# Performance work log

Measured on AMD Instinct MI355X. Metric: run time of the kernel, lower is better.

## Reference

```python
import jax, jax.numpy as jnp
import numpy as np

B, DIM, N_TREES, DEPTH, UNITS = 512, 256, 512, 6, 3
N_LEAVES = 2 ** DEPTH


def binary_lookup_table(depth):
    # (depth, 2**depth, 2) float table of leaf bit codes, as in get_binary_lookup_table
    idx = np.arange(2 ** depth)
    off = 2 ** np.arange(depth)
    bits = (idx[None, :] // off[:, None]) % 2  # (depth, 2**depth)
    lut = np.stack([bits, 1 - bits], axis=-1).astype(np.float32)
    return jnp.asarray(lut)


def sparsemax(z, axis):
    # sparsemax along `axis` (Martins & Astudillo 2016)
    z = jnp.moveaxis(z, axis, -1)
    K = z.shape[-1]
    zs = jnp.flip(jnp.sort(z, axis=-1), axis=-1)
    k = jnp.arange(1, K + 1, dtype=z.dtype)
    cum = jnp.cumsum(zs, axis=-1)
    support = (1.0 + k * zs) > cum
    k_z = jnp.sum(support, axis=-1, keepdims=True)  # int
    tau_num = jnp.take_along_axis(cum, k_z - 1, axis=-1) - 1.0
    tau = tau_num / k_z.astype(z.dtype)
    out = jnp.maximum(z - tau, 0.0)
    return jnp.moveaxis(out, -1, axis)


def sparsemoid(t):
    return jnp.clip(0.5 * t + 0.5, 0.0, 1.0)


def setup_inputs() -> dict:
    key = jax.random.key(0)
    k1, k2, k3, k4 = jax.random.split(key, 4)
    return {
        "x": jax.random.normal(k1, (B, DIM), dtype=jnp.float32),
        "feature_selection_logits": jax.random.normal(k2, (DIM, N_TREES, DEPTH), dtype=jnp.float32),
        "feature_thresholds": jax.random.normal(k3, (N_TREES, DEPTH), dtype=jnp.float32) * 0.5,
        "log_temperatures": jnp.zeros((N_TREES, DEPTH), dtype=jnp.float32),
        "response": jax.random.normal(k4, (N_TREES, UNITS, N_LEAVES), dtype=jnp.float32),
    }


def reference(x, feature_selection_logits, feature_thresholds, log_temperatures, response):
    depth = feature_thresholds.shape[-1]
    lut = binary_lookup_table(depth)  # (d, 2**d, 2) constant
    # soft feature selection: sparsemax over the feature dimension i
    selectors = sparsemax(feature_selection_logits, axis=0)  # (i, n, d)
    fv = jnp.einsum('bi,ind->bnd', x, selectors)  # (b, n, d)
    # binary gates
    tl = (fv - feature_thresholds) * jnp.exp(-log_temperatures)  # (b, n, d)
    gates = sparsemoid(jnp.stack([-tl, tl], axis=-1))  # (b, n, d, 2)
    # leaf aggregation: product over depth of per-level gate selected by the leaf bit code
    agg = jnp.einsum('bnds,dcs->bndc', gates, lut)  # (b, n, d, 2**d)
    leaf_probs = jnp.prod(agg, axis=-2)  # (b, n, 2**d)
    out = jnp.einsum('bnc,nuc->bnu', leaf_probs, response)  # (b, n, units)
    return out
```

## Files before the change

### kernel.cpp

```cpp
#include <hip/hip_runtime.h>
#include <hip/hip_bf16.h>

#define BATCH 512
#define DIM 256
#define NT 512
#define DEPTH 6
#define UNITS 3
#define NL 64
#define COLS (NT * DEPTH)
#define KMAX 32


__global__ __launch_bounds__(256) void k_pack(
    const float* __restrict__ logits, const float* __restrict__ resp,
    const float* __restrict__ thr, const float* __restrict__ ltemp,
    float* __restrict__ logitsT, float4* __restrict__ resp4,
    float* __restrict__ pth, float* __restrict__ pet) {
  const int bid = blockIdx.x, tid = threadIdx.x;
  if (bid < 192) {
    const int c0 = (bid % 48) * 64, r0 = (bid / 48) * 64;
    __shared__ float tile[64][65];
#pragma unroll
    for (int e = tid; e < 4096; e += 256) {
      int r = e >> 6, c = e & 63;
      tile[r][c] = logits[(r0 + r) * COLS + c0 + c];
    }
    __syncthreads();
#pragma unroll
    for (int e = tid; e < 4096; e += 256) {
      int c = e >> 6, r = e & 63;
      logitsT[(c0 + c) * DIM + r0 + r] = tile[r][c];
    }
  } else if (bid < 576) {
    int idx = (bid - 192) * 256 + tid;
    int n = idx / (UNITS * NL);
    int r = idx % (UNITS * NL);
    int u = r / NL, c = r % NL;
    ((float*)&resp4[c * NT + n])[u] = resp[idx];
  } else {
    int idx = (bid - 576) * 256 + tid;
    int n = idx / DEPTH, d = idx % DEPTH;
    pth[d * NT + n] = thr[idx];
    pet[d * NT + n] = expf(-ltemp[idx]);
  }
}

__global__ __launch_bounds__(256) void k_sel(
    const float* __restrict__ logitsT, float4* __restrict__ val4,
    unsigned int* __restrict__ idx4, int* __restrict__ cnt) {
  const int wv = threadIdx.x >> 6, lane = threadIdx.x & 63;
  const int col = blockIdx.x * 4 + wv;
  const int n = col / DEPTH, d = col % DEPTH;

  float z[4];
#pragma unroll
  for (int j = 0; j < 4; ++j) z[j] = logitsT[col * DIM + j * 64 + lane];

  float m = fmaxf(fmaxf(z[0], z[1]), fmaxf(z[2], z[3]));
#pragma unroll
  for (int o = 32; o > 0; o >>= 1) m = fmaxf(m, __shfl_xor(m, o, 64));

  float tau = m - 1.0f;
  for (int it = 0; it < 16; ++it) {
    float s = 0.0f, k = 0.0f;
#pragma unroll
    for (int j = 0; j < 4; ++j) {
      float dd = z[j] - tau;
      if (dd > 0.0f) { s += dd; k += 1.0f; }
    }
#pragma unroll
    for (int o = 32; o > 0; o >>= 1) {
      s += __shfl_xor(s, o, 64);
      k += __shfl_xor(k, o, 64);
    }
    float delta = (s - 1.0f) / k;
    tau += delta;
    if (fabsf(delta) < 1e-7f) break;
  }

  float* vbase = (float*)val4;
  unsigned char* ibase = (unsigned char*)idx4;
  int base = 0;
#pragma unroll
  for (int j = 0; j < 4; ++j) {
    bool nz = z[j] > tau;
    unsigned long long mk = __ballot(nz);
    int pos = base + __popcll(mk & ((1ull << lane) - 1ull));
    if (nz && pos < KMAX) {
      int slot = ((d * 8 + (pos >> 2)) * NT + n) * 4 + (pos & 3);
      vbase[slot] = z[j] - tau;
      ibase[slot] = (unsigned char)(j * 64 + lane);
    }
    base += __popcll(mk);
  }
  const int cc = min(base, KMAX);
  if (lane >= cc && lane < KMAX) {
    int slot = ((d * 8 + (lane >> 2)) * NT + n) * 4 + (lane & 3);
    vbase[slot] = 0.0f;
    ibase[slot] = 0;
  }
  if (lane == 0) cnt[d * NT + n] = cc;
}

__global__ __launch_bounds__(256) void k_forest4(
    const float* __restrict__ x, const float4* __restrict__ val4,
    const unsigned int* __restrict__ idx4, const int* __restrict__ cnt,
    const float* __restrict__ pth, const float* __restrict__ pet,
    const float4* __restrict__ resp4, float* __restrict__ out) {
  const int tid = threadIdx.x;
  const int nloc = tid & 63, bg = tid >> 6;
  const int tt = blockIdx.x & 7, bt = blockIdx.x >> 3;
  const int n = tt * 64 + nloc;
  const int b0 = bt * 8;

  __shared__ float xl[8 * DIM];
#pragma unroll
  for (int k = 0; k < 8; ++k) xl[k * 256 + tid] = x[b0 * DIM + k * 256 + tid];
  __syncthreads();

  const float* xr0 = &xl[(bg * 2 + 0) * DIM];
  const float* xr1 = &xl[(bg * 2 + 1) * DIM];

  float fv0[DEPTH], fv1[DEPTH];
#pragma unroll
  for (int d = 0; d < DEPTH; ++d) { fv0[d] = 0.0f; fv1[d] = 0.0f; }

#pragma unroll
  for (int d = 0; d < DEPTH; ++d) {
    int mc = cnt[d * NT + n];
#pragma unroll
    for (int o = 32; o > 0; o >>= 1) mc = max(mc, __shfl_xor(mc, o, 64));
    const int nq = (mc + 3) >> 2;
#pragma unroll
    for (int jq = 0; jq < 8; ++jq) {
      if (jq < nq) {
        float4 v = val4[(d * 8 + jq) * NT + n];
        unsigned int ip = idx4[(d * 8 + jq) * NT + n];
        int i0 = ip & 255, i1 = (ip >> 8) & 255;
        int i2 = (ip >> 16) & 255, i3 = ip >> 24;
        fv0[d] = fmaf(v.x, xr0[i0], fv0[d]); fv1[d] = fmaf(v.x, xr1[i0], fv1[d]);
        fv0[d] = fmaf(v.y, xr0[i1], fv0[d]); fv1[d] = fmaf(v.y, xr1[i1], fv1[d]);
        fv0[d] = fmaf(v.z, xr0[i2], fv0[d]); fv1[d] = fmaf(v.z, xr1[i2], fv1[d]);
        fv0[d] = fmaf(v.w, xr0[i3], fv0[d]); fv1[d] = fmaf(v.w, xr1[i3], fv1[d]);
      }
    }
  }

  float th[DEPTH], et[DEPTH];
#pragma unroll
  for (int d = 0; d < DEPTH; ++d) {
    th[d] = pth[d * NT + n];
    et[d] = pet[d * NT + n];
  }

  float t012[2][8], t345[2][8];
#pragma unroll
  for (int r = 0; r < 2; ++r) {
    float g0[DEPTH], g1[DEPTH];
#pragma unroll
    for (int d = 0; d < DEPTH; ++d) {
      float av = r ? fv1[d] : fv0[d];
      float tl = (av - th[d]) * et[d];
      float gg = fminf(fmaxf(0.5f * tl + 0.5f, 0.0f), 1.0f);
      g0[d] = gg;
      g1[d] = 1.0f - gg;
    }
#pragma unroll
    for (int c = 0; c < 8; ++c) {
      t012[r][c] = ((c & 1) ? g1[0] : g0[0]) * ((c & 2) ? g1[1] : g0[1]) *
                   ((c & 4) ? g1[2] : g0[2]);
      t345[r][c] = ((c & 1) ? g1[3] : g0[3]) * ((c & 2) ? g1[4] : g0[4]) *
                   ((c & 4) ? g1[5] : g0[5]);
    }
  }

  float o00 = 0, o01 = 0, o02 = 0, o10 = 0, o11 = 0, o12 = 0;
#pragma unroll
  for (int c = 0; c < NL; ++c) {
    float4 rr = resp4[c * NT + n];
    float p0 = t012[0][c & 7] * t345[0][c >> 3];
    float p1 = t012[1][c & 7] * t345[1][c >> 3];
    o00 = fmaf(p0, rr.x, o00); o01 = fmaf(p0, rr.y, o01); o02 = fmaf(p0, rr.z, o02);
    o10 = fmaf(p1, rr.x, o10); o11 = fmaf(p1, rr.y, o11); o12 = fmaf(p1, rr.z, o12);
  }

  const int ba = b0 + bg * 2, bb = ba + 1;
  float* oa = out + ((size_t)ba * NT + n) * UNITS;
  float* ob = out + ((size_t)bb * NT + n) * UNITS;
  oa[0] = o00; oa[1] = o01; oa[2] = o02;
  ob[0] = o10; ob[1] = o11; ob[2] = o12;
}

extern "C" void kernel_launch(void* const* d_in, const int* in_sizes, int n_in,
                              void* d_out, int out_size, void* d_ws, size_t ws_size,
                              hipStream_t stream) {
  const float* x    = (const float*)d_in[0];
  const float* fsl  = (const float*)d_in[1];
  const float* thr  = (const float*)d_in[2];
  const float* lt   = (const float*)d_in[3];
  const float* resp = (const float*)d_in[4];
  float* out = (float*)d_out;

  float* ws = (float*)d_ws;
  float*        logitsT = ws;
  float4*       resp4   = (float4*)(ws + 786432);
  float4*       val4    = (float4*)(ws + 917504);
  unsigned int* idx4    = (unsigned int*)(ws + 1015808);
  int*          cnt     = (int*)(ws + 1040384);
  float*        pth     = ws + 1043456;
  float*        pet     = ws + 1046528;

  k_pack<<<588, 256, 0, stream>>>(fsl, resp, thr, lt, logitsT, resp4, pth, pet);
  k_sel<<<COLS / 4, 256, 0, stream>>>(logitsT, val4, idx4, cnt);
  k_forest4<<<512, 256, 0, stream>>>(x, val4, idx4, cnt, pth, pet, resp4, out);
}
```

Measured before the change: 94.23 us.

## Fuse pack into sparsemax and forest kernels, staging response in shared memory

Removes the separate pack kernel. The sparsemax kernel now transposes the logits through a shared-memory tile itself, and the forest kernel reads thresholds, temperatures and the response table directly, staging the response transposed in LDS. The forest kernel also drops from two batch rows per thread to one and launches twice as many blocks. This cuts one launch and the global round-trips for logitsT and resp4, at the cost of each forest block reloading 48KB of response and recomputing expf per thread.

```diff
diff --git a/kernel.cpp b/kernel.cpp
--- a/kernel.cpp
+++ b/kernel.cpp
@@ -11,119 +11,106 @@
 #define KMAX 32
 
 
-__global__ __launch_bounds__(256) void k_pack(
-    const float* __restrict__ logits, const float* __restrict__ resp,
-    const float* __restrict__ thr, const float* __restrict__ ltemp,
-    float* __restrict__ logitsT, float4* __restrict__ resp4,
-    float* __restrict__ pth, float* __restrict__ pet) {
-  const int bid = blockIdx.x, tid = threadIdx.x;
-  if (bid < 192) {
-    const int c0 = (bid % 48) * 64, r0 = (bid / 48) * 64;
-    __shared__ float tile[64][65];
+__global__ __launch_bounds__(512) void k_sparse(
+    const float* __restrict__ logits, float4* __restrict__ val4,
+    unsigned int* __restrict__ idx4, int* __restrict__ cnt) {
+  const int tid = threadIdx.x;
+  const int c0 = blockIdx.x * 16;
+  __shared__ float tile[16][260];
 #pragma unroll
-    for (int e = tid; e < 4096; e += 256) {
-      int r = e >> 6, c = e & 63;
-      tile[r][c] = logits[(r0 + r) * COLS + c0 + c];
+  for (int it = 0; it < 8; ++it) {
+    int e = it * 512 + tid;
+    int r = e >> 4, c = e & 15;
+    tile[c][r] = logits[r * COLS + c0 + c];
+  }
+  __syncthreads();
+
+  const int wv = tid >> 6, lane = tid & 63;
+  float* vbase = (float*)val4;
+  unsigned char* ibase = (unsigned char*)idx4;
+
+#pragma unroll
+  for (int q = 0; q < 2; ++q) {
+    const int cl = wv * 2 + q;
+    const int col = c0 + cl;
+    const int n = col / DEPTH, d = col % DEPTH;
+
+    float z[4];
+#pragma unroll
+    for (int j = 0; j < 4; ++j) z[j] = tile[cl][j * 64 + lane];
+
+    float m = fmaxf(fmaxf(z[0], z[1]), fmaxf(z[2], z[3]));
+#pragma unroll
+    for (int o = 32; o > 0; o >>= 1) m = fmaxf(m, __shfl_xor(m, o, 64));
+
+    float tau = m - 1.0f;
+    for (int itn = 0; itn < 16; ++itn) {
+      float s = 0.0f, k = 0.0f;
+#pragma unroll
+      for (int j = 0; j < 4; ++j) {
+        float dd = z[j] - tau;
+        if (dd > 0.0f) { s += dd; k += 1.0f; }
+      }
+#pragma unroll
+      for (int o = 32; o > 0; o >>= 1) {
+        s += __shfl_xor(s, o, 64);
+        k += __shfl_xor(k, o, 64);
+      }
+      float delta = (s - 1.0f) / k;
+      tau += delta;
+      if (fabsf(delta) < 1e-7f) break;
     }
-    __syncthreads();
+
+    int base = 0;
 #pragma unroll
-    for (int e = tid; e < 4096; e += 256) {
-      int c = e >> 6, r = e & 63;
-      logitsT[(c0 + c) * DIM + r0 + r] = tile[r][c];
+    for (int j = 0; j < 4; ++j) {
+      bool nz = z[j] > tau;
+      unsigned long long mk = __ballot(nz);
+      int pos = base + __popcll(mk & ((1ull << lane) - 1ull));
+      if (nz && pos < KMAX) {
+        int slot = ((d * 8 + (pos >> 2)) * NT + n) * 4 + (pos & 3);
+        vbase[slot] = z[j] - tau;
+        ibase[slot] = (unsigned char)(j * 64 + lane);
+      }
+      base += __popcll(mk);
     }
-  } else if (bid < 576) {
-    int idx = (bid - 192) * 256 + tid;
-    int n = idx / (UNITS * NL);
-    int r = idx % (UNITS * NL);
-    int u = r / NL, c = r % NL;
-    ((float*)&resp4[c * NT + n])[u] = resp[idx];
-  } else {
-    int idx = (bid - 576) * 256 + tid;
-    int n = idx / DEPTH, d = idx % DEPTH;
-    pth[d * NT + n] = thr[idx];
-    pet[d * NT + n] = expf(-ltemp[idx]);
+    const int cc = min(base, KMAX);
+    if (lane >= cc && lane < KMAX) {
+      int slot = ((d * 8 + (lane >> 2)) * NT + n) * 4 + (lane & 3);
+      vbase[slot] = 0.0f;
+      ibase[slot] = 0;
+    }
+    if (lane == 0) cnt[d * NT + n] = cc;
   }
 }
 
-__global__ __launch_bounds__(256) void k_sel(
-    const float* __restrict__ logitsT, float4* __restrict__ val4,
-    unsigned int* __restrict__ idx4, int* __restrict__ cnt) {
-  const int wv = threadIdx.x >> 6, lane = threadIdx.x & 63;
-  const int col = blockIdx.x * 4 + wv;
-  const int n = col / DEPTH, d = col % DEPTH;
-
-  float z[4];
-#pragma unroll
-  for (int j = 0; j < 4; ++j) z[j] = logitsT[col * DIM + j * 64 + lane];
-
-  float m = fmaxf(fmaxf(z[0], z[1]), fmaxf(z[2], z[3]));
-#pragma unroll
-  for (int o = 32; o > 0; o >>= 1) m = fmaxf(m, __shfl_xor(m, o, 64));
-
-  float tau = m - 1.0f;
-  for (int it = 0; it < 16; ++it) {
-    float s = 0.0f, k = 0.0f;
-#pragma unroll
-    for (int j = 0; j < 4; ++j) {
-      float dd = z[j] - tau;
-      if (dd > 0.0f) { s += dd; k += 1.0f; }
-    }
-#pragma unroll
-    for (int o = 32; o > 0; o >>= 1) {
-      s += __shfl_xor(s, o, 64);
-      k += __shfl_xor(k, o, 64);
-    }
-    float delta = (s - 1.0f) / k;
-    tau += delta;
-    if (fabsf(delta) < 1e-7f) break;
-  }
-
-  float* vbase = (float*)val4;
-  unsigned char* ibase = (unsigned char*)idx4;
-  int base = 0;
-#pragma unroll
-  for (int j = 0; j < 4; ++j) {
-    bool nz = z[j] > tau;
-    unsigned long long mk = __ballot(nz);
-    int pos = base + __popcll(mk & ((1ull << lane) - 1ull));
-    if (nz && pos < KMAX) {
-      int slot = ((d * 8 + (pos >> 2)) * NT + n) * 4 + (pos & 3);
-      vbase[slot] = z[j] - tau;
-      ibase[slot] = (unsigned char)(j * 64 + lane);
-    }
-    base += __popcll(mk);
-  }
-  const int cc = min(base, KMAX);
-  if (lane >= cc && lane < KMAX) {
-    int slot = ((d * 8 + (lane >> 2)) * NT + n) * 4 + (lane & 3);
-    vbase[slot] = 0.0f;
-    ibase[slot] = 0;
-  }
-  if (lane == 0) cnt[d * NT + n] = cc;
-}
-
-__global__ __launch_bounds__(256) void k_forest4(
+__global__ __launch_bounds__(256) void k_forest5(
     const float* __restrict__ x, const float4* __restrict__ val4,
     const unsigned int* __restrict__ idx4, const int* __restrict__ cnt,
-    const float* __restrict__ pth, const float* __restrict__ pet,
-    const float4* __restrict__ resp4, float* __restrict__ out) {
+    const float* __restrict__ thr, const float* __restrict__ ltemp,
+    const float* __restrict__ resp, float* __restrict__ out) {
   const int tid = threadIdx.x;
   const int nloc = tid & 63, bg = tid >> 6;
   const int tt = blockIdx.x & 7, bt = blockIdx.x >> 3;
-  const int n = tt * 64 + nloc;
-  const int b0 = bt * 8;
+  const int n = tt * 64 + nloc, n0 = tt * 64;
+  const int b = bt * 4 + bg;
 
-  __shared__ float xl[8 * DIM];
+  __shared__ float xl[4 * DIM];
+  __shared__ float rsp[UNITS][NL][65];
 #pragma unroll
-  for (int k = 0; k < 8; ++k) xl[k * 256 + tid] = x[b0 * DIM + k * 256 + tid];
+  for (int k2 = 0; k2 < 4; ++k2)
+    xl[k2 * 256 + tid] = x[(bt * 4 + k2) * DIM + tid];
+  for (int k2 = 0; k2 < 48; ++k2) {
+    int e = k2 * 256 + tid;
+    int nl = e / 192, rem = e - nl * 192;
+    rsp[rem >> 6][rem & 63][nl] = resp[n0 * 192 + e];
+  }
   __syncthreads();
 
-  const float* xr0 = &xl[(bg * 2 + 0) * DIM];
-  const float* xr1 = &xl[(bg * 2 + 1) * DIM];
-
-  float fv0[DEPTH], fv1[DEPTH];
+  const float* xr = &xl[bg * DIM];
+  float fv[DEPTH];
 #pragma unroll
-  for (int d = 0; d < DEPTH; ++d) { fv0[d] = 0.0f; fv1[d] = 0.0f; }
+  for (int d = 0; d < DEPTH; ++d) fv[d] = 0.0f;
 
 #pragma unroll
   for (int d = 0; d < DEPTH; ++d) {
@@ -136,59 +123,44 @@
       if (jq < nq) {
         float4 v = val4[(d * 8 + jq) * NT + n];
         unsigned int ip = idx4[(d * 8 + jq) * NT + n];
-        int i0 = ip & 255, i1 = (ip >> 8) & 255;
-        int i2 = (ip >> 16) & 255, i3 = ip >> 24;
-        fv0[d] = fmaf(v.x, xr0[i0], fv0[d]); fv1[d] = fmaf(v.x, xr1[i0], fv1[d]);
-        fv0[d] = fmaf(v.y, xr0[i1], fv0[d]); fv1[d] = fmaf(v.y, xr1[i1], fv1[d]);
-        fv0[d] = fmaf(v.z, xr0[i2], fv0[d]); fv1[d] = fmaf(v.z, xr1[i2], fv1[d]);
-        fv0[d] = fmaf(v.w, xr0[i3], fv0[d]); fv1[d] = fmaf(v.w, xr1[i3], fv1[d]);
+        fv[d] = fmaf(v.x, xr[ip & 255], fv[d]);
+        fv[d] = fmaf(v.y, xr[(ip >> 8) & 255], fv[d]);
+        fv[d] = fmaf(v.z, xr[(ip >> 16) & 255], fv[d]);
+        fv[d] = fmaf(v.w, xr[ip >> 24], fv[d]);
       }
     }
   }
 
-  float th[DEPTH], et[DEPTH];
-#pragma unroll
-  for (int d = 0; d < DEPTH; ++d) {
-    th[d] = pth[d * NT + n];
-    et[d] = pet[d * NT + n];
-  }
-
-  float t012[2][8], t345[2][8];
-#pragma unroll
-  for (int r = 0; r < 2; ++r) {
+  float t012[8], t345[8];
+  {
     float g0[DEPTH], g1[DEPTH];
 #pragma unroll
     for (int d = 0; d < DEPTH; ++d) {
-      float av = r ? fv1[d] : fv0[d];
-      float tl = (av - th[d]) * et[d];
+      float tl = (fv[d] - thr[n * DEPTH + d]) * expf(-ltemp[n * DEPTH + d]);
       float gg = fminf(fmaxf(0.5f * tl + 0.5f, 0.0f), 1.0f);
       g0[d] = gg;
       g1[d] = 1.0f - gg;
     }
 #pragma unroll
     for (int c = 0; c < 8; ++c) {
-      t012[r][c] = ((c & 1) ? g1[0] : g0[0]) * ((c & 2) ? g1[1] : g0[1]) *
-                   ((c & 4) ? g1[2] : g0[2]);
-      t345[r][c] = ((c & 1) ? g1[3] : g0[3]) * ((c & 2) ? g1[4] : g0[4]) *
-                   ((c & 4) ? g1[5] : g0[5]);
+      t012[c] = ((c & 1) ? g1[0] : g0[0]) * ((c & 2) ? g1[1] : g0[1]) *
+                ((c & 4) ? g1[2] : g0[2]);
+      t345[c] = ((c & 1) ? g1[3] : g0[3]) * ((c & 2) ? g1[4] : g0[4]) *
+                ((c & 4) ? g1[5] : g0[5]);
     }
   }
 
-  float o00 = 0, o01 = 0, o02 = 0, o10 = 0, o11 = 0, o12 = 0;
+  float o0 = 0.0f, o1 = 0.0f, o2 = 0.0f;
 #pragma unroll
   for (int c = 0; c < NL; ++c) {
-    float4 rr = resp4[c * NT + n];
-    float p0 = t012[0][c & 7] * t345[0][c >> 3];
-    float p1 = t012[1][c & 7] * t345[1][c >> 3];
-    o00 = fmaf(p0, rr.x, o00); o01 = fmaf(p0, rr.y, o01); o02 = fmaf(p0, rr.z, o02);
-    o10 = fmaf(p1, rr.x, o10); o11 = fmaf(p1, rr.y, o11); o12 = fmaf(p1, rr.z, o12);
+    float p = t012[c & 7] * t345[c >> 3];
+    o0 = fmaf(p, rsp[0][c][nloc], o0);
+    o1 = fmaf(p, rsp[1][c][nloc], o1);
+    o2 = fmaf(p, rsp[2][c][nloc], o2);
   }
 
-  const int ba = b0 + bg * 2, bb = ba + 1;
-  float* oa = out + ((size_t)ba * NT + n) * UNITS;
-  float* ob = out + ((size_t)bb * NT + n) * UNITS;
-  oa[0] = o00; oa[1] = o01; oa[2] = o02;
-  ob[0] = o10; ob[1] = o11; ob[2] = o12;
+  float* op = out + ((size_t)b * NT + n) * UNITS;
+  op[0] = o0; op[1] = o1; op[2] = o2;
 }
 
 extern "C" void kernel_launch(void* const* d_in, const int* in_sizes, int n_in,
@@ -202,15 +174,10 @@
   float* out = (float*)d_out;
 
   float* ws = (float*)d_ws;
-  float*        logitsT = ws;
-  float4*       resp4   = (float4*)(ws + 786432);
-  float4*       val4    = (float4*)(ws + 917504);
-  unsigned int* idx4    = (unsigned int*)(ws + 1015808);
-  int*          cnt     = (int*)(ws + 1040384);
-  float*        pth     = ws + 1043456;
-  float*        pet     = ws + 1046528;
+  float4*       val4 = (float4*)ws;
+  unsigned int* idx4 = (unsigned int*)(ws + 98304);
+  int*          cnt  = (int*)(ws + 122880);
 
-  k_pack<<<588, 256, 0, stream>>>(fsl, resp, thr, lt, logitsT, resp4, pth, pet);
-  k_sel<<<COLS / 4, 256, 0, stream>>>(logitsT, val4, idx4, cnt);
-  k_forest4<<<512, 256, 0, stream>>>(x, val4, idx4, cnt, pth, pet, resp4, out);
+  k_sparse<<<COLS / 16, 512, 0, stream>>>(fsl, val4, idx4, cnt);
+  k_forest5<<<1024, 256, 0, stream>>>(x, val4, idx4, cnt, thr, lt, resp, out);
 }
```

New measurement: 98.94 us. 1.05x slower.

## Fuse transpose with sparsemax selection and store responses as bf16

Applied to the files above, without the earlier changes.

Merges the logits transpose and the sparsemax selection into a single prep kernel. Each block now loads its 8 columns through shared memory, so the logitsT round-trip through global memory and one kernel launch go away. Response weights are stored as packed bf16 (uint2 instead of float4), which halves that read in the forest kernel. The count-driven early exit is removed so all 8 quads are always processed, which adds some work on zero-padded entries. The bf16 responses reduce precision of the final output.

```diff
diff --git a/kernel.cpp b/kernel.cpp
--- a/kernel.cpp
+++ b/kernel.cpp
@@ -11,102 +11,120 @@
 #define KMAX 32
 
 
-__global__ __launch_bounds__(256) void k_pack(
+__device__ __forceinline__ unsigned short f2bf(float f) {
+  unsigned int u = __float_as_uint(f);
+  return (unsigned short)((u + 0x7fffu + ((u >> 16) & 1u)) >> 16);
+}
+
+__global__ __launch_bounds__(512) void k_prep6(
     const float* __restrict__ logits, const float* __restrict__ resp,
     const float* __restrict__ thr, const float* __restrict__ ltemp,
-    float* __restrict__ logitsT, float4* __restrict__ resp4,
-    float* __restrict__ pth, float* __restrict__ pet) {
+    float4* __restrict__ val4, unsigned int* __restrict__ idx4,
+    uint2* __restrict__ respB, float* __restrict__ pth,
+    float* __restrict__ pet) {
   const int bid = blockIdx.x, tid = threadIdx.x;
-  if (bid < 192) {
-    const int c0 = (bid % 48) * 64, r0 = (bid / 48) * 64;
-    __shared__ float tile[64][65];
-#pragma unroll
-    for (int e = tid; e < 4096; e += 256) {
-      int r = e >> 6, c = e & 63;
-      tile[r][c] = logits[(r0 + r) * COLS + c0 + c];
+  __shared__ float tile[8][260];
+  __shared__ float lds[64 * 196];
+
+  if (bid < 384) {
+    const int c0 = bid * 8;
+#pragma unroll
+    for (int it = 0; it < 4; ++it) {
+      int e = it * 512 + tid;
+      int r = e >> 3, c = e & 7;
+      tile[c][r] = logits[r * COLS + c0 + c];
     }
     __syncthreads();
-#pragma unroll
-    for (int e = tid; e < 4096; e += 256) {
-      int c = e >> 6, r = e & 63;
-      logitsT[(c0 + c) * DIM + r0 + r] = tile[r][c];
-    }
-  } else if (bid < 576) {
-    int idx = (bid - 192) * 256 + tid;
-    int n = idx / (UNITS * NL);
-    int r = idx % (UNITS * NL);
-    int u = r / NL, c = r % NL;
-    ((float*)&resp4[c * NT + n])[u] = resp[idx];
+
+    const int wv = tid >> 6, lane = tid & 63;
+    const int col = c0 + wv;
+    const int n = col / DEPTH, d = col % DEPTH;
+
+    float z[4];
+#pragma unroll
+    for (int j = 0; j < 4; ++j) z[j] = tile[wv][j * 64 + lane];
+
+    float m = fmaxf(fmaxf(z[0], z[1]), fmaxf(z[2], z[3]));
+#pragma unroll
+    for (int o = 32; o > 0; o >>= 1) m = fmaxf(m, __shfl_xor(m, o, 64));
+
+    float tau = m - 1.0f;
+    for (int itn = 0; itn < 16; ++itn) {
+      float s = 0.0f, k = 0.0f;
+#pragma unroll
+      for (int j = 0; j < 4; ++j) {
+        float dd = z[j] - tau;
+        if (dd > 0.0f) { s += dd; k += 1.0f; }
+      }
+#pragma unroll
+      for (int o = 32; o > 0; o >>= 1) {
+        s += __shfl_xor(s, o, 64);
+        k += __shfl_xor(k, o, 64);
+      }
+      float delta = (s - 1.0f) / k;
+      tau += delta;
+      if (fabsf(delta) < 1e-7f) break;
+    }
+
+    float* vbase = (float*)val4;
+    unsigned char* ibase = (unsigned char*)idx4;
+    int base = 0;
+#pragma unroll
+    for (int j = 0; j < 4; ++j) {
+      bool nz = z[j] > tau;
+      unsigned long long mk = __ballot(nz);
+      int pos = base + __popcll(mk & ((1ull << lane) - 1ull));
+      if (nz && pos < KMAX) {
+        int slot = ((d * 8 + (pos >> 2)) * NT + n) * 4 + (pos & 3);
+        vbase[slot] = z[j] - tau;
+        ibase[slot] = (unsigned char)(j * 64 + lane);
+      }
+      base += __popcll(mk);
+    }
+    const int cc = min(base, KMAX);
+    if (lane >= cc && lane < KMAX) {
+      int slot = ((d * 8 + (lane >> 2)) * NT + n) * 4 + (lane & 3);
+      vbase[slot] = 0.0f;
+      ibase[slot] = 0;
+    }
+  } else if (bid < 392) {
+    const int n0 = (bid - 384) * 64;
+    const float4* r4 = (const float4*)(resp + n0 * 192);
+#pragma unroll
+    for (int k = 0; k < 6; ++k) {
+      int f4 = k * 512 + tid;
+      float4 v = r4[f4];
+      int nl = f4 / 48, rem = (f4 % 48) * 4;
+      float* p = &lds[nl * 196 + rem];
+      p[0] = v.x; p[1] = v.y; p[2] = v.z; p[3] = v.w;
+    }
+    __syncthreads();
+#pragma unroll
+    for (int k = 0; k < 8; ++k) {
+      int s = k * 512 + tid;
+      int c = s >> 6, nl = s & 63;
+      unsigned int b0 = f2bf(lds[nl * 196 + 0 * 64 + c]);
+      unsigned int b1 = f2bf(lds[nl * 196 + 1 * 64 + c]);
+      unsigned int b2 = f2bf(lds[nl * 196 + 2 * 64 + c]);
+      respB[c * NT + n0 + nl] = make_uint2(b0 | (b1 << 16), b2);
+    }
   } else {
-    int idx = (bid - 576) * 256 + tid;
-    int n = idx / DEPTH, d = idx % DEPTH;
-    pth[d * NT + n] = thr[idx];
-    pet[d * NT + n] = expf(-ltemp[idx]);
-  }
-}
-
-__global__ __launch_bounds__(256) void k_sel(
-    const float* __restrict__ logitsT, float4* __restrict__ val4,
-    unsigned int* __restrict__ idx4, int* __restrict__ cnt) {
-  const int wv = threadIdx.x >> 6, lane = threadIdx.x & 63;
-  const int col = blockIdx.x * 4 + wv;
-  const int n = col / DEPTH, d = col % DEPTH;
-
-  float z[4];
-#pragma unroll
-  for (int j = 0; j < 4; ++j) z[j] = logitsT[col * DIM + j * 64 + lane];
-
-  float m = fmaxf(fmaxf(z[0], z[1]), fmaxf(z[2], z[3]));
-#pragma unroll
-  for (int o = 32; o > 0; o >>= 1) m = fmaxf(m, __shfl_xor(m, o, 64));
-
-  float tau = m - 1.0f;
-  for (int it = 0; it < 16; ++it) {
-    float s = 0.0f, k = 0.0f;
-#pragma unroll
-    for (int j = 0; j < 4; ++j) {
-      float dd = z[j] - tau;
-      if (dd > 0.0f) { s += dd; k += 1.0f; }
-    }
-#pragma unroll
-    for (int o = 32; o > 0; o >>= 1) {
-      s += __shfl_xor(s, o, 64);
-      k += __shfl_xor(k, o, 64);
-    }
-    float delta = (s - 1.0f) / k;
-    tau += delta;
-    if (fabsf(delta) < 1e-7f) break;
-  }
-
-  float* vbase = (float*)val4;
-  unsigned char* ibase = (unsigned char*)idx4;
-  int base = 0;
-#pragma unroll
-  for (int j = 0; j < 4; ++j) {
-    bool nz = z[j] > tau;
-    unsigned long long mk = __ballot(nz);
-    int pos = base + __popcll(mk & ((1ull << lane) - 1ull));
-    if (nz && pos < KMAX) {
-      int slot = ((d * 8 + (pos >> 2)) * NT + n) * 4 + (pos & 3);
-      vbase[slot] = z[j] - tau;
-      ibase[slot] = (unsigned char)(j * 64 + lane);
-    }
-    base += __popcll(mk);
-  }
-  const int cc = min(base, KMAX);
-  if (lane >= cc && lane < KMAX) {
-    int slot = ((d * 8 + (lane >> 2)) * NT + n) * 4 + (lane & 3);
-    vbase[slot] = 0.0f;
-    ibase[slot] = 0;
-  }
-  if (lane == 0) cnt[d * NT + n] = cc;
-}
-
-__global__ __launch_bounds__(256) void k_forest4(
+    int i = (bid - 392) * 512 + tid;
+#pragma unroll
+    for (int k = 0; k < 3; ++k) {
+      int idx = k * 1024 + i;
+      int n = idx / DEPTH, d = idx % DEPTH;
+      pth[d * NT + n] = thr[idx];
+      pet[d * NT + n] = expf(-ltemp[idx]);
+    }
+  }
+}
+
+__global__ __launch_bounds__(256) void k_forest6(
     const float* __restrict__ x, const float4* __restrict__ val4,
-    const unsigned int* __restrict__ idx4, const int* __restrict__ cnt,
-    const float* __restrict__ pth, const float* __restrict__ pet,
-    const float4* __restrict__ resp4, float* __restrict__ out) {
+    const unsigned int* __restrict__ idx4, const float* __restrict__ pth,
+    const float* __restrict__ pet, const uint2* __restrict__ respB,
+    float* __restrict__ out) {
   const int tid = threadIdx.x;
   const int nloc = tid & 63, bg = tid >> 6;
   const int tt = blockIdx.x & 7, bt = blockIdx.x >> 3;
@@ -127,30 +145,17 @@
 
 #pragma unroll
   for (int d = 0; d < DEPTH; ++d) {
-    int mc = cnt[d * NT + n];
-#pragma unroll
-    for (int o = 32; o > 0; o >>= 1) mc = max(mc, __shfl_xor(mc, o, 64));
-    const int nq = (mc + 3) >> 2;
 #pragma unroll
     for (int jq = 0; jq < 8; ++jq) {
-      if (jq < nq) {
-        float4 v = val4[(d * 8 + jq) * NT + n];
-        unsigned int ip = idx4[(d * 8 + jq) * NT + n];
-        int i0 = ip & 255, i1 = (ip >> 8) & 255;
-        int i2 = (ip >> 16) & 255, i3 = ip >> 24;
-        fv0[d] = fmaf(v.x, xr0[i0], fv0[d]); fv1[d] = fmaf(v.x, xr1[i0], fv1[d]);
-        fv0[d] = fmaf(v.y, xr0[i1], fv0[d]); fv1[d] = fmaf(v.y, xr1[i1], fv1[d]);
-        fv0[d] = fmaf(v.z, xr0[i2], fv0[d]); fv1[d] = fmaf(v.z, xr1[i2], fv1[d]);
-        fv0[d] = fmaf(v.w, xr0[i3], fv0[d]); fv1[d] = fmaf(v.w, xr1[i3], fv1[d]);
-      }
-    }
-  }
-
-  float th[DEPTH], et[DEPTH];
-#pragma unroll
-  for (int d = 0; d < DEPTH; ++d) {
-    th[d] = pth[d * NT + n];
-    et[d] = pet[d * NT + n];
+      float4 v = val4[(d * 8 + jq) * NT + n];
+      unsigned int ip = idx4[(d * 8 + jq) * NT + n];
+      int i0 = ip & 255, i1 = (ip >> 8) & 255;
+      int i2 = (ip >> 16) & 255, i3 = ip >> 24;
+      fv0[d] = fmaf(v.x, xr0[i0], fv0[d]); fv1[d] = fmaf(v.x, xr1[i0], fv1[d]);
+      fv0[d] = fmaf(v.y, xr0[i1], fv0[d]); fv1[d] = fmaf(v.y, xr1[i1], fv1[d]);
+      fv0[d] = fmaf(v.z, xr0[i2], fv0[d]); fv1[d] = fmaf(v.z, xr1[i2], fv1[d]);
+      fv0[d] = fmaf(v.w, xr0[i3], fv0[d]); fv1[d] = fmaf(v.w, xr1[i3], fv1[d]);
+    }
   }
 
   float t012[2][8], t345[2][8];
@@ -160,7 +165,7 @@
 #pragma unroll
     for (int d = 0; d < DEPTH; ++d) {
       float av = r ? fv1[d] : fv0[d];
-      float tl = (av - th[d]) * et[d];
+      float tl = (av - pth[d * NT + n]) * pet[d * NT + n];
       float gg = fminf(fmaxf(0.5f * tl + 0.5f, 0.0f), 1.0f);
       g0[d] = gg;
       g1[d] = 1.0f - gg;
@@ -177,11 +182,14 @@
   float o00 = 0, o01 = 0, o02 = 0, o10 = 0, o11 = 0, o12 = 0;
 #pragma unroll
   for (int c = 0; c < NL; ++c) {
-    float4 rr = resp4[c * NT + n];
+    uint2 rb = respB[c * NT + n];
+    float r0 = __uint_as_float(rb.x << 16);
+    float r1 = __uint_as_float(rb.x & 0xffff0000u);
+    float r2 = __uint_as_float(rb.y << 16);
     float p0 = t012[0][c & 7] * t345[0][c >> 3];
     float p1 = t012[1][c & 7] * t345[1][c >> 3];
-    o00 = fmaf(p0, rr.x, o00); o01 = fmaf(p0, rr.y, o01); o02 = fmaf(p0, rr.z, o02);
-    o10 = fmaf(p1, rr.x, o10); o11 = fmaf(p1, rr.y, o11); o12 = fmaf(p1, rr.z, o12);
+    o00 = fmaf(p0, r0, o00); o01 = fmaf(p0, r1, o01); o02 = fmaf(p0, r2, o02);
+    o10 = fmaf(p1, r0, o10); o11 = fmaf(p1, r1, o11); o12 = fmaf(p1, r2, o12);
   }
 
   const int ba = b0 + bg * 2, bb = ba + 1;
@@ -202,15 +210,12 @@
   float* out = (float*)d_out;
 
   float* ws = (float*)d_ws;
-  float*        logitsT = ws;
-  float4*       resp4   = (float4*)(ws + 786432);
-  float4*       val4    = (float4*)(ws + 917504);
-  unsigned int* idx4    = (unsigned int*)(ws + 1015808);
-  int*          cnt     = (int*)(ws + 1040384);
-  float*        pth     = ws + 1043456;
-  float*        pet     = ws + 1046528;
-
-  k_pack<<<588, 256, 0, stream>>>(fsl, resp, thr, lt, logitsT, resp4, pth, pet);
-  k_sel<<<COLS / 4, 256, 0, stream>>>(logitsT, val4, idx4, cnt);
-  k_forest4<<<512, 256, 0, stream>>>(x, val4, idx4, cnt, pth, pet, resp4, out);
-}
+  float4*       val4  = (float4*)ws;
+  unsigned int* idx4  = (unsigned int*)(ws + 98304);
+  uint2*        respB = (uint2*)(ws + 122880);
+  float*        pth   = ws + 188416;
+  float*        pet   = ws + 191488;
+
+  k_prep6<<<394, 512, 0, stream>>>(fsl, resp, thr, lt, val4, idx4, respB, pth, pet);
+  k_forest6<<<512, 256, 0, stream>>>(x, val4, idx4, pth, pet, respB, out);
+}
```

Result: faster. 85.84 us (-8.9%).
